# Kernel optimization log

Measured on AMD Instinct MI355X. Metric: run time of the kernel, lower is better.

## Reference

```python
import jax, jax.numpy as jnp
import numpy as np

D = 128            # dim_h
EDIM = D + 108     # tgt emb + 108-way edge one-hot (edge_linear in_features)
NSRC = 10000       # candidate source nodes
NEDGE = 320000     # candidate paths (edges), ~32 per src
TOPN = 6           # top_n path selection
GIN_EPS = 0.0      # init_eps, not learned
BN_EPS = 1e-5


def _batch_norm(x, gamma, beta):
    # torch BatchNorm1d in training mode: batch stats, biased variance
    mean = jnp.mean(x, axis=0)
    var = jnp.var(x, axis=0)
    return gamma * (x - mean) * jax.lax.rsqrt(var + BN_EPS) + beta


def _glorot(key, shape):
    fan_in, fan_out = shape[-2], shape[-1]
    lim = np.sqrt(6.0 / (fan_in + fan_out))
    return jax.random.uniform(key, shape, jnp.float32, -lim, lim)


def setup_inputs() -> dict:
    key = jax.random.key(0)
    ks = jax.random.split(key, 24)
    inp = {
        "paths_srcs": jax.random.normal(ks[0], (NSRC, D), jnp.float32),
        "path_feats": jax.random.normal(ks[1], (NEDGE, EDIM), jnp.float32),
        "src_ids": jax.random.randint(ks[2], (NEDGE,), 0, NSRC, jnp.int32),
        # 3 stacked GIN convs (weights stacked on leading axis)
        "conv_edge_W": _glorot(ks[3], (3, EDIM, D)),
        "conv_edge_b": jnp.zeros((3, D), jnp.float32),
        "conv_W1": _glorot(ks[4], (3, D, D)),       # MLP layer1, no bias
        "conv_bn_g": jnp.ones((3, D), jnp.float32),
        "conv_bn_b": jnp.zeros((3, D), jnp.float32),
        "conv_W2": _glorot(ks[5], (3, D, D)),       # MLP layer2, no bias
        # GINStack heads
        "lin1_W": _glorot(ks[6], (3 * D, D)),
        "lin1_b": jnp.zeros((D,), jnp.float32),
        "lin2_W": _glorot(ks[7], (D, D)),
        "lin2_b": jnp.zeros((D,), jnp.float32),
        # PathEncoder
        "pe_src_W": _glorot(ks[8], (D, D)),
        "pe_src_b": jnp.zeros((D,), jnp.float32),
        "pe_tgt_W": _glorot(ks[9], (EDIM, D)),
        "pe_tgt_b": jnp.zeros((D,), jnp.float32),
        "pe_bn_g": jnp.ones((D,), jnp.float32),
        "pe_bn_b": jnp.zeros((D,), jnp.float32),
        # linear path ranker head
        "score_w": _glorot(ks[10], (D, 1))[:, 0],
    }
    return inp


def reference(paths_srcs, path_feats, conv_edge_W, conv_edge_b, conv_W1,
              conv_bn_g, conv_bn_b, conv_W2, lin1_W, lin1_b, lin2_W, lin2_b,
              pe_src_W, pe_src_b, pe_tgt_W, pe_tgt_b, pe_bn_g, pe_bn_b,
              score_w, src_ids):
    # GIN message: relu(tgt+edge feature), summed per source node.
    # Identical for all 3 convs in the original, so compute once.
    msgs = jax.nn.relu(path_feats)                                   # [E, EDIM]
    agg = jax.ops.segment_sum(msgs, src_ids, num_segments=NSRC)      # [N, EDIM]

    hs = []
    for i in range(3):  # fixed 3-layer GINStack
        h_msg = agg @ conv_edge_W[i] + conv_edge_b[i]                # [N, D]
        h = (1.0 + GIN_EPS) * paths_srcs + h_msg
        z = jax.nn.relu(_batch_norm(h @ conv_W1[i], conv_bn_g[i], conv_bn_b[i]))
        hs.append(z @ conv_W2[i])
    h = jnp.concatenate(hs, axis=1) @ lin1_W + lin1_b                # [N, D]
    h = jax.nn.relu(h)
    node_emb = h @ lin2_W + lin2_b                                   # [N, D]

    # PathEncoder: src-node emb + fused (tgt+edge) emb -> path emb
    hpath = node_emb[src_ids] @ pe_src_W + pe_src_b \
          + path_feats @ pe_tgt_W + pe_tgt_b                         # [E, D]
    hpath = jax.nn.relu(_batch_norm(hpath, pe_bn_g, pe_bn_b))

    # linear path ranker + top-k path selection
    scores = hpath @ score_w                                         # [E]
    top_vals, top_idx = jax.lax.top_k(scores, TOPN)
    return node_emb, top_vals, top_idx
```

## Files before the change

kernel.cpp:

```cpp
#include <hip/hip_runtime.h>
#include <math.h>

#define NSRC 10000
#define NEDGE 320000
#define EDIM 236
#define TOPN 6

typedef __attribute__((ext_vector_type(8))) short short8;
typedef __attribute__((ext_vector_type(4))) float floatx4;

__device__ __forceinline__ unsigned short bf16_rne(float x) {
  union { float f; unsigned int u; } c; c.f = x;
  unsigned int r = (c.u + 0x7FFFu + ((c.u >> 16) & 1u)) >> 16;
  return (unsigned short)r;
}
__device__ __forceinline__ float bf16_to_f(unsigned short h) {
  union { unsigned int u; float f; } c; c.u = ((unsigned int)h) << 16;
  return c.f;
}
__device__ __forceinline__ void split_f32(float x, unsigned short& h, unsigned short& l) {
  h = bf16_rne(x);
  l = bf16_rne(x - bf16_to_f(h));
}

struct KV { float v; int i; };

__device__ __forceinline__ bool kv_better(const KV a, const KV b) {
  return (a.v > b.v) || (a.v == b.v && a.i < b.i);
}

__device__ __forceinline__ void kv_merge(KV d[TOPN], const KV o[TOPN]) {
  KV r[TOPN];
  int ia = 0, ib = 0;
#pragma unroll
  for (int q = 0; q < TOPN; ++q) {
    bool takeA;
    if (ia >= TOPN) takeA = false;
    else if (ib >= TOPN) takeA = true;
    else takeA = kv_better(d[ia], o[ib]);
    r[q] = takeA ? d[ia] : o[ib];
    if (takeA) ia++; else ib++;
  }
#pragma unroll
  for (int q = 0; q < TOPN; ++q) d[q] = r[q];
}

__global__ void k_sentinel(float* __restrict__ out) {
  if (threadIdx.x == 0) out[0] = 1.0e9f;
}

__global__ __launch_bounds__(256)
void k_prep_all(const float* __restrict__ cew, const float* __restrict__ ceb,
                const float* __restrict__ cw1, const float* __restrict__ cw2,
                const float* __restrict__ l1w, const float* __restrict__ l2w,
                const float* __restrict__ psw, const float* __restrict__ l2b,
                const float* __restrict__ psb, const float* __restrict__ ptb,
                const float* __restrict__ ptw,
                float* __restrict__ w1cat, float* __restrict__ wew1cat,
                float* __restrict__ bprime, float* __restrict__ m1,
                unsigned short* __restrict__ Bh, unsigned short* __restrict__ Bl,
                float* __restrict__ bcat, float* __restrict__ biascat,
                float* __restrict__ statsT, int* __restrict__ counts) {
  const int b = blockIdx.x;
  const int tid = threadIdx.x;
  if (b < 708) {
    if (tid >= 128) return;
    int i = b / EDIM;
    int k = b - i * EDIM;
    const float* we = cew + ((size_t)i * EDIM + k) * 128;
    const float* w1 = cw1 + (size_t)i * 16384;
    float acc = 0.f;
    for (int m = 0; m < 128; ++m) acc = fmaf(we[m], w1[m * 128 + tid], acc);
    wew1cat[k * 384 + i * 128 + tid] = acc;
  } else if (b < 1092) {
    if (tid >= 128) return;
    int bb = b - 708;
    int i = bb >> 7;
    int r = bb & 127;
    const float* w2 = cw2 + (size_t)i * 16384 + r * 128;
    float acc = 0.f;
    for (int c = 0; c < 128; ++c) acc = fmaf(w2[c], l1w[((size_t)i * 128 + c) * 128 + tid], acc);
    m1[bb * 128 + tid] = acc;
  } else if (b < 1284) {
    int gid = (b - 1092) * 256 + tid;
    if (gid >= 3 * 128 * 128) return;
    int i = gid >> 14;
    int m = (gid >> 7) & 127;
    int j = gid & 127;
    w1cat[m * 384 + i * 128 + j] = cw1[gid];
  } else if (b < 1287) {
    if (tid >= 128) return;
    int i = b - 1284;
    const float* be = ceb + i * 128;
    const float* w1 = cw1 + (size_t)i * 16384;
    float acc = 0.f;
    for (int m = 0; m < 128; ++m) acc = fmaf(be[m], w1[m * 128 + tid], acc);
    bprime[i * 128 + tid] = acc;
  } else if (b < 1415) {
    int n = b - 1287;
    float v = (tid < EDIM) ? ptw[(size_t)tid * 128 + n] : 0.f;
    unsigned short h, l;
    split_f32(v, h, l);
    Bh[n * 256 + tid] = h;
    Bl[n * 256 + tid] = l;
  } else if (b < 1543) {
    if (tid >= 128) return;
    int k = b - 1415;
    bcat[k * 256 + tid] = l2w[k * 128 + tid];
    float acc = 0.f;
    for (int c = 0; c < 128; ++c) acc = fmaf(l2w[k * 128 + c], psw[c * 128 + tid], acc);
    bcat[k * 256 + 128 + tid] = acc;
    if (k == 0) {
      biascat[tid] = l2b[tid];
      float bb = 0.f;
      for (int c = 0; c < 128; ++c) bb = fmaf(l2b[c], psw[c * 128 + tid], bb);
      biascat[128 + tid] = bb + psb[tid] + ptb[tid];
    }
  } else if (b < 1551) {
    int i = (b - 1543) * 256 + tid;
    if (i < 2048) statsT[i] = 0.f;
  } else {
    int i = (b - 1551) * 256 + tid;
    if (i < NSRC) counts[i] = 0;
  }
}

__global__ __launch_bounds__(256) void k_hist(const int* __restrict__ src,
                                              int* __restrict__ counts) {
  int e = blockIdx.x * 256 + threadIdx.x;
  if (e < NEDGE) atomicAdd(&counts[src[e]], 1);
}

__global__ __launch_bounds__(256) void k_scan(const int* __restrict__ counts,
                                              int* __restrict__ offsets,
                                              int* __restrict__ cursor) {
  __shared__ int part[256];
  const int t = threadIdx.x;
  const int base = t * 40;
  int s = 0;
  for (int k = 0; k < 40; ++k) {
    int i = base + k;
    if (i < NSRC) s += counts[i];
  }
  part[t] = s;
  __syncthreads();
  for (int off = 1; off < 256; off <<= 1) {
    int v = (t >= off) ? part[t - off] : 0;
    __syncthreads();
    part[t] += v;
    __syncthreads();
  }
  int run = (t == 0) ? 0 : part[t - 1];
  for (int k = 0; k < 40; ++k) {
    int i = base + k;
    if (i < NSRC) {
      offsets[i] = run;
      cursor[i] = run;
      run += counts[i];
    }
  }
  if (t == 255) offsets[NSRC] = run;
}

__global__ __launch_bounds__(256) void k_scatter(const int* __restrict__ src,
                                                 int* __restrict__ cursor,
                                                 int* __restrict__ elist) {
  int e = blockIdx.x * 256 + threadIdx.x;
  if (e < NEDGE) {
    int p = atomicAdd(&cursor[src[e]], 1);
    elist[p] = e;
  }
}

__global__ __launch_bounds__(256) void k_gather(const float* __restrict__ pf,
                                                const int* __restrict__ offsets,
                                                const int* __restrict__ elist,
                                                float* __restrict__ agg) {
  const int row = blockIdx.x;
  const int t = threadIdx.x;
  __shared__ int sid[64];
  const int beg = offsets[row];
  const int end = offsets[row + 1];
  float a[8];
#pragma unroll
  for (int q = 0; q < 8; ++q) a[q] = 0.f;
  for (int b = beg; b < end; b += 64) {
    const int cnt = min(64, end - b);
    __syncthreads();
    if (t < cnt) sid[t] = elist[b + t];
    __syncthreads();
    if (t < EDIM) {
      int e = 0;
      for (; e + 8 <= cnt; e += 8) {
        int i0 = sid[e], i1 = sid[e + 1], i2 = sid[e + 2], i3 = sid[e + 3];
        int i4 = sid[e + 4], i5 = sid[e + 5], i6 = sid[e + 6], i7 = sid[e + 7];
        a[0] += fmaxf(pf[(size_t)i0 * EDIM + t], 0.f);
        a[1] += fmaxf(pf[(size_t)i1 * EDIM + t], 0.f);
        a[2] += fmaxf(pf[(size_t)i2 * EDIM + t], 0.f);
        a[3] += fmaxf(pf[(size_t)i3 * EDIM + t], 0.f);
        a[4] += fmaxf(pf[(size_t)i4 * EDIM + t], 0.f);
        a[5] += fmaxf(pf[(size_t)i5 * EDIM + t], 0.f);
        a[6] += fmaxf(pf[(size_t)i6 * EDIM + t], 0.f);
        a[7] += fmaxf(pf[(size_t)i7 * EDIM + t], 0.f);
      }
      for (; e < cnt; ++e) a[0] += fmaxf(pf[(size_t)sid[e] * EDIM + t], 0.f);
    }
  }
  if (t < EDIM)
    agg[(size_t)row * EDIM + t] =
        ((a[0] + a[1]) + (a[2] + a[3])) + ((a[4] + a[5]) + (a[6] + a[7]));
}

__global__ __launch_bounds__(256)
void k_gemmT(const float* __restrict__ A1, const float* __restrict__ B1,
             const float* __restrict__ A2, const float* __restrict__ B2,
             const float* __restrict__ bias, float* __restrict__ C,
             float* __restrict__ colsum, float* __restrict__ colsumsq) {
  __shared__ float As[8][64];
  __shared__ float Bs[8][64];
  __shared__ float red[16][64];
  const int tid = threadIdx.x;
  const int tx = tid & 15;
  const int ty = tid >> 4;
  const int bm = blockIdx.x * 64;
  const int bn = blockIdx.y * 64;
  const int N = 384;

  float acc[4][4];
#pragma unroll
  for (int i = 0; i < 4; ++i)
#pragma unroll
    for (int j = 0; j < 4; ++j) acc[i][j] = 0.f;

  const int ar = tid & 63;
  const int ac = (tid >> 6) << 1;
  const int bkr = tid >> 5;
  const int bc = (tid & 31) << 1;

#pragma unroll 1
  for (int seg = 0; seg < 2; ++seg) {
    const float* A = seg ? A2 : A1;
    const float* B = seg ? B2 : B1;
    const int K = seg ? EDIM : 128;
    for (int k0 = 0; k0 < K; k0 += 8) {
      {
        float2 v = make_float2(0.f, 0.f);
        int row = bm + ar;
        int k = k0 + ac;
        if (row < NSRC) {
          if (k + 2 <= K) v = *(const float2*)(A + (size_t)row * K + k);
          else if (k < K) v.x = A[(size_t)row * K + k];
        }
        As[ac][ar] = v.x;
        As[ac + 1][ar] = v.y;
      }
      {
        float2 v = make_float2(0.f, 0.f);
        int kk = k0 + bkr;
        if (kk < K) v = *(const float2*)(B + (size_t)kk * N + bn + bc);
        Bs[bkr][bc] = v.x;
        Bs[bkr][bc + 1] = v.y;
      }
      __syncthreads();
#pragma unroll
      for (int kk = 0; kk < 8; ++kk) {
        const float4 a0 = *(const float4*)&As[kk][ty * 4];
        const float4 b0 = *(const float4*)&Bs[kk][tx * 4];
        const float av[4] = {a0.x, a0.y, a0.z, a0.w};
        const float bv[4] = {b0.x, b0.y, b0.z, b0.w};
#pragma unroll
        for (int i = 0; i < 4; ++i)
#pragma unroll
          for (int j = 0; j < 4; ++j) acc[i][j] = fmaf(av[i], bv[j], acc[i][j]);
      }
      __syncthreads();
    }
  }

  const int nb = bn + tx * 4;
  float colS[4], colQ[4];
#pragma unroll
  for (int j = 0; j < 4; ++j) { colS[j] = 0.f; colQ[j] = 0.f; }
#pragma unroll
  for (int i = 0; i < 4; ++i) {
    int m = bm + ty * 4 + i;
    if (m < NSRC) {
      float outv[4];
#pragma unroll
      for (int j = 0; j < 4; ++j) outv[j] = acc[i][j] + bias[nb + j];
      *(float4*)(C + (size_t)m * N + nb) = make_float4(outv[0], outv[1], outv[2], outv[3]);
#pragma unroll
      for (int j = 0; j < 4; ++j) { colS[j] += outv[j]; colQ[j] += outv[j] * outv[j]; }
    }
  }
  *(float4*)&red[ty][tx * 4] = make_float4(colS[0], colS[1], colS[2], colS[3]);
  __syncthreads();
  if (tid < 64) {
    float s = 0.f;
#pragma unroll
    for (int t = 0; t < 16; ++t) s += red[t][tid];
    atomicAdd(colsum + bn + tid, s);
  }
  __syncthreads();
  *(float4*)&red[ty][tx * 4] = make_float4(colQ[0], colQ[1], colQ[2], colQ[3]);
  __syncthreads();
  if (tid < 64) {
    float s = 0.f;
#pragma unroll
    for (int t = 0; t < 16; ++t) s += red[t][tid];
    atomicAdd(colsumsq + bn + tid, s);
  }
}

template <int ATR, int EPI>
__global__ __launch_bounds__(256)
void gemm_k(const float* __restrict__ A, const float* __restrict__ B,
            float* __restrict__ C, int M, int K, int N,
            const float* __restrict__ bn_g, const float* __restrict__ bn_b,
            const float* __restrict__ rawS, const float* __restrict__ rawQ,
            const float* __restrict__ bias, float* __restrict__ C2) {
  __shared__ float As[8][64];
  __shared__ float Bs[8][64];
  const int tid = threadIdx.x;
  const int tx = tid & 15;
  const int ty = tid >> 4;
  const int bm = blockIdx.x * 64;
  const int bn = blockIdx.y * 64;

  float acc[4][4];
#pragma unroll
  for (int i = 0; i < 4; ++i)
#pragma unroll
    for (int j = 0; j < 4; ++j) acc[i][j] = 0.f;

  const int ar = tid & 63;
  const int ac = (tid >> 6) << 1;
  const int bkr = tid >> 5;
  const int bc = (tid & 31) << 1;

  for (int k0 = 0; k0 < K; k0 += 8) {
    {
      float2 v = make_float2(0.f, 0.f);
      int row = bm + ar;
      int k = k0 + ac;
      if (row < M) {
        if (k + 2 <= K) v = *(const float2*)(A + (size_t)row * K + k);
        else if (k < K) v.x = A[(size_t)row * K + k];
      }
      if constexpr (ATR == 2) {
        float vv[2] = {v.x, v.y};
#pragma unroll
        for (int q = 0; q < 2; ++q) {
          int kk = k0 + ac + q;
          if (kk < K) {
            float mean = rawS[kk] * (1.0f / NSRC);
            float var = rawQ[kk] * (1.0f / NSRC) - mean * mean;
            float rstd = rsqrtf(var + 1e-5f);
            vv[q] = fmaxf(fmaf(bn_g[kk] * rstd, vv[q] - mean, bn_b[kk]), 0.f);
          } else {
            vv[q] = 0.f;
          }
        }
        v = make_float2(vv[0], vv[1]);
      }
      As[ac][ar] = v.x;
      As[ac + 1][ar] = v.y;
    }
    {
      float2 v = make_float2(0.f, 0.f);
      int kk = k0 + bkr;
      if (kk < K) v = *(const float2*)(B + (size_t)kk * N + bn + bc);
      Bs[bkr][bc] = v.x;
      Bs[bkr][bc + 1] = v.y;
    }
    __syncthreads();
#pragma unroll
    for (int kk = 0; kk < 8; ++kk) {
      const float4 a0 = *(const float4*)&As[kk][ty * 4];
      const float4 b0 = *(const float4*)&Bs[kk][tx * 4];
      const float av[4] = {a0.x, a0.y, a0.z, a0.w};
      const float bv[4] = {b0.x, b0.y, b0.z, b0.w};
#pragma unroll
      for (int i = 0; i < 4; ++i)
#pragma unroll
        for (int j = 0; j < 4; ++j) acc[i][j] = fmaf(av[i], bv[j], acc[i][j]);
    }
    __syncthreads();
  }

  const int nb = bn + tx * 4;
#pragma unroll
  for (int i = 0; i < 4; ++i) {
    int m = bm + ty * 4 + i;
    if (m < M) {
      float outv[4];
#pragma unroll
      for (int j = 0; j < 4; ++j) {
        outv[j] = acc[i][j] + bias[nb + j];
        if constexpr (EPI == 2) outv[j] = fmaxf(outv[j], 0.f);
      }
      float* crow;
      if constexpr (EPI == 5) {
        crow = (nb < 128) ? (C + (size_t)m * 128 + nb) : (C2 + (size_t)m * 128 + (nb - 128));
      } else {
        crow = C + (size_t)m * N + nb;
      }
      *(float4*)crow = make_float4(outv[0], outv[1], outv[2], outv[3]);
    }
  }
}

__global__ __launch_bounds__(256)
void k_hgemm(const float* __restrict__ A, const unsigned short* __restrict__ Bh,
             const unsigned short* __restrict__ Bl, const int* __restrict__ srcids,
             const float* __restrict__ pre_src, float* __restrict__ hpath,
             float* __restrict__ colsum, float* __restrict__ colsumsq) {
  __shared__ __align__(16) unsigned short Bhs[128][40];
  __shared__ __align__(16) unsigned short Bls[128][40];
  __shared__ float redS[4][128];
  __shared__ float redQ[4][128];

  const int tid = threadIdx.x;
  const int wave = tid >> 6;
  const int lane = tid & 63;
  const int am = lane & 15;
  const int aq = lane >> 4;
  const int bm = blockIdx.x * 128;

  floatx4 acc[2][8];
#pragma unroll
  for (int mt = 0; mt < 2; ++mt)
#pragma unroll
    for (int nt = 0; nt < 8; ++nt) acc[mt][nt] = (floatx4){0.f, 0.f, 0.f, 0.f};

  const int rowS = tid >> 1;
  const int kq = (tid & 1) * 16;
  const float* a0p = A + (size_t)(bm + wave * 32 + am) * EDIM;
  const float* a1p = a0p + 16 * EDIM;
  const unsigned short* bhp0 = Bh + (size_t)rowS * 256 + kq;
  const unsigned short* blp0 = Bl + (size_t)rowS * 256 + kq;

  short8 pBh0, pBh1, pBl0, pBl1;
  float pA0[8], pA1[8];

  auto loadB = [&](int c) {
    const unsigned short* bhp = bhp0 + c * 32;
    const unsigned short* blp = blp0 + c * 32;
    pBh0 = *(const short8*)bhp;
    pBh1 = *(const short8*)(bhp + 8);
    pBl0 = *(const short8*)blp;
    pBl1 = *(const short8*)(blp + 8);
  };
  auto loadA = [&](int c) {
    const int kA = c * 32 + aq * 8;
    if (kA + 8 <= EDIM) {
      float4 x = *(const float4*)(a0p + kA);
      float4 y = *(const float4*)(a0p + kA + 4);
      pA0[0] = x.x; pA0[1] = x.y; pA0[2] = x.z; pA0[3] = x.w;
      pA0[4] = y.x; pA0[5] = y.y; pA0[6] = y.z; pA0[7] = y.w;
      x = *(const float4*)(a1p + kA);
      y = *(const float4*)(a1p + kA + 4);
      pA1[0] = x.x; pA1[1] = x.y; pA1[2] = x.z; pA1[3] = x.w;
      pA1[4] = y.x; pA1[5] = y.y; pA1[6] = y.z; pA1[7] = y.w;
    } else {
#pragma unroll
      for (int q = 0; q < 8; ++q) {
        int k = kA + q;
        pA0[q] = (k < EDIM) ? a0p[k] : 0.f;
        pA1[q] = (k < EDIM) ? a1p[k] : 0.f;
      }
    }
  };

  loadB(0);
  loadA(0);
#pragma unroll
  for (int c = 0; c < 8; ++c) {
    *(short8*)&Bhs[rowS][kq] = pBh0;
    *(short8*)&Bhs[rowS][kq + 8] = pBh1;
    *(short8*)&Bls[rowS][kq] = pBl0;
    *(short8*)&Bls[rowS][kq + 8] = pBl1;
    short8 ah0, al0, ah1, al1;
#pragma unroll
    for (int q = 0; q < 8; ++q) {
      unsigned short h, l;
      split_f32(pA0[q], h, l);
      ah0[q] = (short)h; al0[q] = (short)l;
      split_f32(pA1[q], h, l);
      ah1[q] = (short)h; al1[q] = (short)l;
    }
    __syncthreads();
    if (c < 7) {
      loadB(c + 1);
      loadA(c + 1);
    }
#pragma unroll
    for (int nt = 0; nt < 8; ++nt) {
      const short8 bh = *(const short8*)&Bhs[nt * 16 + am][aq * 8];
      const short8 bl = *(const short8*)&Bls[nt * 16 + am][aq * 8];
      acc[0][nt] = __builtin_amdgcn_mfma_f32_16x16x32_bf16(ah0, bl, acc[0][nt], 0, 0, 0);
      acc[1][nt] = __builtin_amdgcn_mfma_f32_16x16x32_bf16(ah1, bl, acc[1][nt], 0, 0, 0);
      acc[0][nt] = __builtin_amdgcn_mfma_f32_16x16x32_bf16(al0, bh, acc[0][nt], 0, 0, 0);
      acc[1][nt] = __builtin_amdgcn_mfma_f32_16x16x32_bf16(al1, bh, acc[1][nt], 0, 0, 0);
      acc[0][nt] = __builtin_amdgcn_mfma_f32_16x16x32_bf16(ah0, bh, acc[0][nt], 0, 0, 0);
      acc[1][nt] = __builtin_amdgcn_mfma_f32_16x16x32_bf16(ah1, bh, acc[1][nt], 0, 0, 0);
    }
    __syncthreads();
  }

  float colS[8], colQ[8];
#pragma unroll
  for (int nt = 0; nt < 8; ++nt) { colS[nt] = 0.f; colQ[nt] = 0.f; }
#pragma unroll
  for (int mt = 0; mt < 2; ++mt) {
#pragma unroll
    for (int r = 0; r < 4; ++r) {
      const int m = bm + wave * 32 + mt * 16 + aq * 4 + r;
      const int sid = srcids[m];
      const float* g = pre_src + (size_t)sid * 128;
      float* hp = hpath + (size_t)m * 128;
#pragma unroll
      for (int nt = 0; nt < 8; ++nt) {
        const int col = nt * 16 + am;
        float v = acc[mt][nt][r] + g[col];
        hp[col] = v;
        colS[nt] += v;
        colQ[nt] += v * v;
      }
    }
  }
#pragma unroll
  for (int nt = 0; nt < 8; ++nt) {
    colS[nt] += __shfl_xor(colS[nt], 16);
    colS[nt] += __shfl_xor(colS[nt], 32);
    colQ[nt] += __shfl_xor(colQ[nt], 16);
    colQ[nt] += __shfl_xor(colQ[nt], 32);
  }
  if (lane < 16) {
#pragma unroll
    for (int nt = 0; nt < 8; ++nt) {
      redS[wave][nt * 16 + lane] = colS[nt];
      redQ[wave][nt * 16 + lane] = colQ[nt];
    }
  }
  __syncthreads();
  if (tid < 128) {
    float s = redS[0][tid] + redS[1][tid] + redS[2][tid] + redS[3][tid];
    atomicAdd(colsum + tid, s);
  } else {
    int cn = tid - 128;
    float s = redQ[0][cn] + redQ[1][cn] + redQ[2][cn] + redQ[3][cn];
    atomicAdd(colsumsq + cn, s);
  }
}

__global__ __launch_bounds__(256)
void k_scoretop(const float* __restrict__ hpath, const float* __restrict__ stP,
                const float* __restrict__ g, const float* __restrict__ b,
                const float* __restrict__ w, KV* __restrict__ cand) {
  const int tid = threadIdx.x;
  const int cg = tid & 15;
  const int grp = (blockIdx.x * 256 + tid) >> 4;
  float a8[8], c8[8], w8[8];
#pragma unroll
  for (int q = 0; q < 8; ++q) {
    int j = cg * 8 + q;
    float mean = stP[j] * (1.0f / NEDGE);
    float var = stP[128 + j] * (1.0f / NEDGE) - mean * mean;
    float rstd = rsqrtf(var + 1e-5f);
    float aj = g[j] * rstd;
    a8[q] = aj;
    c8[q] = b[j] - aj * mean;
    w8[q] = w[j];
  }
  KV t[TOPN];
#pragma unroll
  for (int q = 0; q < TOPN; ++q) { t[q].v = -INFINITY; t[q].i = 2147483647; }
  for (int row = grp; row < NEDGE; row += 16384) {
    const float* hp = hpath + (size_t)row * 128 + cg * 8;
    const float4 x0 = *(const float4*)hp;
    const float4 x1 = *(const float4*)(hp + 4);
    const float xs[8] = {x0.x, x0.y, x0.z, x0.w, x1.x, x1.y, x1.z, x1.w};
    float part = 0.f;
#pragma unroll
    for (int q = 0; q < 8; ++q)
      part += fmaxf(fmaf(a8[q], xs[q], c8[q]), 0.f) * w8[q];
#pragma unroll
    for (int o = 8; o >= 1; o >>= 1) part += __shfl_xor(part, o, 16);
    if (cg == 0 && part > t[TOPN - 1].v) {
      t[TOPN - 1].v = part;
      t[TOPN - 1].i = row;
#pragma unroll
      for (int q = TOPN - 1; q > 0; --q) {
        if (t[q].v > t[q - 1].v) { KV tmp = t[q - 1]; t[q - 1] = t[q]; t[q] = tmp; }
      }
    }
  }
  __shared__ KV sh[128][TOPN];
  for (int s = 128; s >= 1; s >>= 1) {
    if (tid >= s && tid < 2 * s) {
#pragma unroll
      for (int q = 0; q < TOPN; ++q) sh[tid - s][q] = t[q];
    }
    __syncthreads();
    if (tid < s) kv_merge(t, sh[tid]);
    __syncthreads();
  }
  if (tid == 0) {
#pragma unroll
    for (int q = 0; q < TOPN; ++q) cand[blockIdx.x * TOPN + q] = t[q];
  }
}

__global__ __launch_bounds__(256) void k_top2(const KV* __restrict__ cand,
                                              float* __restrict__ outTail) {
  int tid = threadIdx.x;
  KV t[TOPN];
#pragma unroll
  for (int q = 0; q < TOPN; ++q) t[q] = cand[tid * TOPN + q];
  for (int gset = 1; gset < 4; ++gset) {
    KV o[TOPN];
#pragma unroll
    for (int q = 0; q < TOPN; ++q) o[q] = cand[(gset * 256 + tid) * TOPN + q];
    kv_merge(t, o);
  }
  __shared__ KV sh[128][TOPN];
  for (int s = 128; s >= 1; s >>= 1) {
    if (tid >= s && tid < 2 * s) {
#pragma unroll
      for (int q = 0; q < TOPN; ++q) sh[tid - s][q] = t[q];
    }
    __syncthreads();
    if (tid < s) kv_merge(t, sh[tid]);
    __syncthreads();
  }
  if (tid == 0) {
#pragma unroll
    for (int q = 0; q < TOPN; ++q) {
      outTail[q] = t[q].v;
      outTail[TOPN + q] = (float)t[q].i;
    }
  }
}

extern "C" void kernel_launch(void* const* d_in, const int* in_sizes, int n_in,
                              void* d_out, int out_size, void* d_ws, size_t ws_size,
                              hipStream_t stream) {
  const float* paths_srcs = (const float*)d_in[0];
  const float* path_feats = (const float*)d_in[1];
  const int* src_ids = (const int*)d_in[2];
  const float* cew = (const float*)d_in[3];
  const float* ceb = (const float*)d_in[4];
  const float* cw1 = (const float*)d_in[5];
  const float* bng = (const float*)d_in[6];
  const float* bnbt = (const float*)d_in[7];
  const float* cw2 = (const float*)d_in[8];
  const float* l1w = (const float*)d_in[9];
  const float* l1b = (const float*)d_in[10];
  const float* l2w = (const float*)d_in[11];
  const float* l2b = (const float*)d_in[12];
  const float* psw = (const float*)d_in[13];
  const float* psb = (const float*)d_in[14];
  const float* ptw = (const float*)d_in[15];
  const float* ptb = (const float*)d_in[16];
  const float* pbg = (const float*)d_in[17];
  const float* pbb = (const float*)d_in[18];
  const float* scw = (const float*)d_in[19];
  float* out = (float*)d_out;
  float* ws = (float*)d_ws;

  float* w1cat = ws;
  float* wew1cat = w1cat + 49152;
  float* bprime = wew1cat + 90624;
  float* m1 = bprime + 512;
  float* statsT = m1 + 49152;
  float* statsP = statsT + 1536;
  float* agg = statsP + 512;
  float* T = agg + 2360000;
  float* H1 = T + 3840000;
  float* pre_src = H1 + 1280000;
  float* scores_dead = pre_src + 1280000;
  float* candpad = scores_dead + 320000;
  float* hpath = candpad + 3072;
  unsigned short* Bh = (unsigned short*)(hpath + 40960000);
  unsigned short* Bl = Bh + 32768;
  float* bcat = (float*)(Bl + 32768);
  float* biascat = bcat + 32768;
  KV* cand = (KV*)scores_dead;
  int* counts = (int*)hpath;
  int* offsets = counts + 10000;
  int* cursor = offsets + 10001;
  int* elist = cursor + 10000;
  const size_t needed = (size_t)(49152 + 90624 + 512 + 49152 + 1536 + 512 + 2360000 +
                                 3840000 + 1280000 + 1280000 + 320000 + 3072 +
                                 40960000 + 16384 + 16384 + 32768 + 256) * 4;
  if (ws_size < needed) {
    k_sentinel<<<1, 64, 0, stream>>>(out);
    return;
  }

  k_prep_all<<<1591, 256, 0, stream>>>(cew, ceb, cw1, cw2, l1w, l2w, psw, l2b, psb, ptb,
                                       ptw, w1cat, wew1cat, bprime, m1, Bh, Bl,
                                       bcat, biascat, statsT, counts);
  k_hist<<<(NEDGE + 255) / 256, 256, 0, stream>>>(src_ids, counts);
  k_scan<<<1, 256, 0, stream>>>(counts, offsets, cursor);
  k_scatter<<<(NEDGE + 255) / 256, 256, 0, stream>>>(src_ids, cursor, elist);
  k_gather<<<NSRC, 256, 0, stream>>>(path_feats, offsets, elist, agg);
  k_gemmT<<<dim3(157, 6), 256, 0, stream>>>(paths_srcs, w1cat, agg, wew1cat, bprime, T,
                                            statsT, statsT + 384);
  gemm_k<2, 2><<<dim3(157, 2), 256, 0, stream>>>(T, m1, H1, NSRC, 384, 128,
                                                 bng, bnbt, statsT, statsT + 384,
                                                 l1b, nullptr);
  gemm_k<0, 5><<<dim3(157, 4), 256, 0, stream>>>(H1, bcat, out, NSRC, 128, 256,
                                                 nullptr, nullptr, nullptr, nullptr,
                                                 biascat, pre_src);
  k_hgemm<<<2500, 256, 0, stream>>>(path_feats, Bh, Bl, src_ids, pre_src, hpath,
                                    statsP, statsP + 128);
  k_scoretop<<<1024, 256, 0, stream>>>(hpath, statsP, pbg, pbb, scw, cand);
  k_top2<<<1, 256, 0, stream>>>(cand, out + (size_t)NSRC * 128);
}
```

Before: 968.6 us.

## Stage hgemm B tiles via direct global-to-LDS loads with double buffering

The E-row path GEMM kernel now copies the split-bf16 weight tiles straight from global memory into LDS with global_load_lds. It uses two LDS buffers in a fragment-ordered layout, so each lane reads its MFMA operand contiguously and the second barrier per k-step is dropped. The fp32-to-bf16 hi/lo split of the A operand now uses packed v_cvt_pk_bf16_f32 instructions instead of scalar rounding. The main loop is no longer unrolled, and the single barrier must still order the async LDS writes against reads of the other buffer.

```diff
diff --git a/kernel.cpp b/kernel.cpp
--- a/kernel.cpp
+++ b/kernel.cpp
@@ -9,6 +9,13 @@
 typedef __attribute__((ext_vector_type(8))) short short8;
 typedef __attribute__((ext_vector_type(4))) float floatx4;
 
+typedef __attribute__((address_space(3))) void lds_void_t;
+typedef __attribute__((address_space(1))) const void gmem_void_t;
+
+__device__ __forceinline__ void g2lds16(const void* g, void* l) {
+  __builtin_amdgcn_global_load_lds((gmem_void_t*)g, (lds_void_t*)l, 16, 0, 0);
+}
+
 __device__ __forceinline__ unsigned short bf16_rne(float x) {
   union { float f; unsigned int u; } c; c.f = x;
   unsigned int r = (c.u + 0x7FFFu + ((c.u >> 16) & 1u)) >> 16;
@@ -21,6 +28,24 @@
 __device__ __forceinline__ void split_f32(float x, unsigned short& h, unsigned short& l) {
   h = bf16_rne(x);
   l = bf16_rne(x - bf16_to_f(h));
+}
+
+__device__ __forceinline__ void split8(const float* av, short8& h8, short8& l8) {
+  union { short8 s; unsigned int u[4]; } H, L;
+#pragma unroll
+  for (int p = 0; p < 4; ++p) {
+    float x0 = av[2 * p], x1 = av[2 * p + 1];
+    unsigned int hp;
+    asm("v_cvt_pk_bf16_f32 %0, %1, %2" : "=v"(hp) : "v"(x0), "v"(x1));
+    union { unsigned int u; float f; } f0, f1;
+    f0.u = hp << 16;
+    f1.u = hp & 0xFFFF0000u;
+    float l0 = x0 - f0.f, l1 = x1 - f1.f;
+    unsigned int lp;
+    asm("v_cvt_pk_bf16_f32 %0, %1, %2" : "=v"(lp) : "v"(l0), "v"(l1));
+    H.u[p] = hp; L.u[p] = lp;
+  }
+  h8 = H.s; l8 = L.s;
 }
 
 struct KV { float v; int i; };
@@ -415,8 +440,7 @@
              const unsigned short* __restrict__ Bl, const int* __restrict__ srcids,
              const float* __restrict__ pre_src, float* __restrict__ hpath,
              float* __restrict__ colsum, float* __restrict__ colsumsq) {
-  __shared__ __align__(16) unsigned short Bhs[128][40];
-  __shared__ __align__(16) unsigned short Bls[128][40];
+  __shared__ __align__(16) unsigned short BF[2][2][8][512];
   __shared__ float redS[4][128];
   __shared__ float redQ[4][128];
 
@@ -433,24 +457,23 @@
 #pragma unroll
     for (int nt = 0; nt < 8; ++nt) acc[mt][nt] = (floatx4){0.f, 0.f, 0.f, 0.f};
 
-  const int rowS = tid >> 1;
-  const int kq = (tid & 1) * 16;
   const float* a0p = A + (size_t)(bm + wave * 32 + am) * EDIM;
   const float* a1p = a0p + 16 * EDIM;
-  const unsigned short* bhp0 = Bh + (size_t)rowS * 256 + kq;
-  const unsigned short* blp0 = Bl + (size_t)rowS * 256 + kq;
-
-  short8 pBh0, pBh1, pBl0, pBl1;
+
+  const int nt0 = wave * 2, nt1 = nt0 + 1;
+  const unsigned short* sH0 = Bh + (size_t)(nt0 * 16 + am) * 256 + aq * 8;
+  const unsigned short* sH1 = Bh + (size_t)(nt1 * 16 + am) * 256 + aq * 8;
+  const unsigned short* sL0 = Bl + (size_t)(nt0 * 16 + am) * 256 + aq * 8;
+  const unsigned short* sL1 = Bl + (size_t)(nt1 * 16 + am) * 256 + aq * 8;
+
+  auto stage = [&](int c, int buf) {
+    g2lds16(sH0 + c * 32, &BF[buf][0][nt0][0]);
+    g2lds16(sH1 + c * 32, &BF[buf][0][nt1][0]);
+    g2lds16(sL0 + c * 32, &BF[buf][1][nt0][0]);
+    g2lds16(sL1 + c * 32, &BF[buf][1][nt1][0]);
+  };
+
   float pA0[8], pA1[8];
-
-  auto loadB = [&](int c) {
-    const unsigned short* bhp = bhp0 + c * 32;
-    const unsigned short* blp = blp0 + c * 32;
-    pBh0 = *(const short8*)bhp;
-    pBh1 = *(const short8*)(bhp + 8);
-    pBl0 = *(const short8*)blp;
-    pBl1 = *(const short8*)(blp + 8);
-  };
   auto loadA = [&](int c) {
     const int kA = c * 32 + aq * 8;
     if (kA + 8 <= EDIM) {
@@ -472,32 +495,23 @@
     }
   };
 
-  loadB(0);
+  stage(0, 0);
   loadA(0);
-#pragma unroll
+#pragma unroll 1
   for (int c = 0; c < 8; ++c) {
-    *(short8*)&Bhs[rowS][kq] = pBh0;
-    *(short8*)&Bhs[rowS][kq + 8] = pBh1;
-    *(short8*)&Bls[rowS][kq] = pBl0;
-    *(short8*)&Bls[rowS][kq + 8] = pBl1;
     short8 ah0, al0, ah1, al1;
-#pragma unroll
-    for (int q = 0; q < 8; ++q) {
-      unsigned short h, l;
-      split_f32(pA0[q], h, l);
-      ah0[q] = (short)h; al0[q] = (short)l;
-      split_f32(pA1[q], h, l);
-      ah1[q] = (short)h; al1[q] = (short)l;
-    }
+    split8(pA0, ah0, al0);
+    split8(pA1, ah1, al1);
     __syncthreads();
     if (c < 7) {
-      loadB(c + 1);
+      stage(c + 1, (c + 1) & 1);
       loadA(c + 1);
     }
+    const int buf = c & 1;
 #pragma unroll
     for (int nt = 0; nt < 8; ++nt) {
-      const short8 bh = *(const short8*)&Bhs[nt * 16 + am][aq * 8];
-      const short8 bl = *(const short8*)&Bls[nt * 16 + am][aq * 8];
+      const short8 bh = *(const short8*)&BF[buf][0][nt][lane * 8];
+      const short8 bl = *(const short8*)&BF[buf][1][nt][lane * 8];
       acc[0][nt] = __builtin_amdgcn_mfma_f32_16x16x32_bf16(ah0, bl, acc[0][nt], 0, 0, 0);
       acc[1][nt] = __builtin_amdgcn_mfma_f32_16x16x32_bf16(ah1, bl, acc[1][nt], 0, 0, 0);
       acc[0][nt] = __builtin_amdgcn_mfma_f32_16x16x32_bf16(al0, bh, acc[0][nt], 0, 0, 0);
@@ -505,7 +519,6 @@
       acc[0][nt] = __builtin_amdgcn_mfma_f32_16x16x32_bf16(ah0, bh, acc[0][nt], 0, 0, 0);
       acc[1][nt] = __builtin_amdgcn_mfma_f32_16x16x32_bf16(ah1, bh, acc[1][nt], 0, 0, 0);
     }
-    __syncthreads();
   }
 
   float colS[8], colQ[8];
```

Measured after the change: 916.2 us, median of 2. 5.4% less time.
